# Optimization experiments

Measured on AMD Instinct MI355X. Metric: run time of the kernel, lower is better.

Reference implementation:

```python
import jax, jax.numpy as jnp
import numpy as np

N_NODES = 100000
N_EDGES = 1600000
IN_DIM = 128
HEADS = 4
HEAD_DIM = 16  # hidden_dim 64 // 4 heads
HID = HEADS * HEAD_DIM
NEG_SLOPE = 0.2


def setup_inputs() -> dict:
    key = jax.random.key(0)
    ks = jax.random.split(key, 20)
    inp = {
        "x": jax.random.normal(ks[0], (N_NODES, IN_DIM), dtype=jnp.float32),
        "edge_index": jax.random.randint(ks[1], (2, N_EDGES), 0, N_NODES, dtype=jnp.int32),
    }
    dims = [IN_DIM, HID, HID]
    for l in range(3):
        d_in = dims[l]
        sc = 1.0 / np.sqrt(d_in)
        inp[f"w{l}"] = jax.random.normal(ks[2 + 4 * l], (d_in, HID), dtype=jnp.float32) * sc
        inp[f"asrc{l}"] = jax.random.normal(ks[3 + 4 * l], (HEADS, HEAD_DIM), dtype=jnp.float32) * 0.1
        inp[f"adst{l}"] = jax.random.normal(ks[4 + 4 * l], (HEADS, HEAD_DIM), dtype=jnp.float32) * 0.1
        inp[f"b{l}"] = jnp.zeros((HID,), dtype=jnp.float32)
    inp["out_w"] = jax.random.normal(ks[14], (HID, 1), dtype=jnp.float32) * (1.0 / np.sqrt(HID))
    inp["out_b"] = jnp.zeros((1,), dtype=jnp.float32)
    return inp


def _gat_layer(h, src, dst, W, a_src, a_dst, b):
    # h: [N, d_in]; src/dst: [E'] (self-loops already appended)
    n = h.shape[0]
    xh = (h @ W).reshape(n, HEADS, HEAD_DIM)              # [N,H,C]
    al_s = jnp.sum(xh * a_src, axis=-1)                   # [N,H]
    al_d = jnp.sum(xh * a_dst, axis=-1)                   # [N,H]
    e = jax.nn.leaky_relu(al_s[src] + al_d[dst], NEG_SLOPE)  # [E',H]
    # segment-softmax over incoming edges of each destination node
    m = jax.ops.segment_max(e, dst, num_segments=n)       # [N,H]
    p = jnp.exp(e - m[dst])
    z = jax.ops.segment_sum(p, dst, num_segments=n)       # [N,H]
    alpha = p / (z[dst] + 1e-16)                          # [E',H]
    msg = xh[src] * alpha[:, :, None]                     # [E',H,C]
    out = jax.ops.segment_sum(msg, dst, num_segments=n)   # [N,H,C]
    return out.reshape(n, HID) + b


def reference(x, edge_index, w0, asrc0, adst0, b0, w1, asrc1, adst1, b1,
              w2, asrc2, adst2, b2, out_w, out_b):
    n = x.shape[0]
    loops = jnp.arange(n, dtype=edge_index.dtype)
    src = jnp.concatenate([edge_index[0], loops])  # PyG GATConv adds self-loops
    dst = jnp.concatenate([edge_index[1], loops])
    h = x
    params = [(w0, asrc0, adst0, b0), (w1, asrc1, adst1, b1), (w2, asrc2, adst2, b2)]
    for W, a_s, a_d, b in params:
        h = _gat_layer(h, src, dst, W, a_s, a_d, b)
        h = jax.nn.relu(h)
    return (h @ out_w + out_b).squeeze(-1)  # [N]
```

## Files before the change

kernel.cpp:

```cpp
#include <hip/hip_runtime.h>


#define NBMAX 512
#define SCHUNK 4096
#define BCAP 8192
#define PADSLACK 768

typedef __attribute__((ext_vector_type(8))) short bf16x8;
typedef __attribute__((ext_vector_type(4))) float f32x4;

__device__ inline unsigned short bf16_rtn(float x) {
    union { float f; unsigned u; } a; a.f = x;
    return (unsigned short)((a.u + 0x7FFFu + ((a.u >> 16) & 1u)) >> 16);
}
__device__ inline float bf16_to_f(unsigned short s) {
    union { unsigned u; float f; } b; b.u = ((unsigned)s) << 16;
    return b.f;
}

__global__ __launch_bounds__(256) void k_init(int* __restrict__ bhist, int nb,
                                              float* __restrict__ als, float* __restrict__ xh, int n) {
    int i = blockIdx.x * 256 + threadIdx.x;
    if (i < nb) bhist[i] = 0;
    int j = i - NBMAX;
    if (j >= 0 && j < 4) als[(size_t)n * 4 + j] = -1e30f;
    int k = i - NBMAX - 4;
    if (k >= 0 && k < 64) xh[(size_t)n * 64 + k] = 0.f;
}

__global__ __launch_bounds__(256) void k_bhist(const int* __restrict__ dst, int* __restrict__ bhist, int e) {
    __shared__ unsigned int h[NBMAX];
    int t = threadIdx.x;
    h[t] = 0;
    h[t + 256] = 0;
    __syncthreads();
    for (int i = blockIdx.x * 256 + t; i < e; i += gridDim.x * 256)
        atomicAdd(&h[dst[i] >> 8], 1u);
    __syncthreads();
    if (h[t]) atomicAdd(&bhist[t], (int)h[t]);
    if (h[t + 256]) atomicAdd(&bhist[t + 256], (int)h[t + 256]);
}

__global__ __launch_bounds__(512) void k_bscan(const int* __restrict__ bhist, int* __restrict__ boffs,
                                               int* __restrict__ bfill, int nb, int e) {
    __shared__ int s[NBMAX];
    int t = threadIdx.x;
    int v = (t < nb) ? bhist[t] : 0;
    s[t] = v;
    __syncthreads();
    for (int o = 1; o < 512; o <<= 1) {
        int add = (t >= o) ? s[t - o] : 0;
        __syncthreads();
        s[t] += add;
        __syncthreads();
    }
    boffs[t] = s[t] - v;
    if (t == 511) boffs[512] = s[511];
    bfill[t] = 0;
}

__global__ __launch_bounds__(512) void k_bscatter(const int* __restrict__ src, const int* __restrict__ dst,
                                                  const int* __restrict__ boffs, int* __restrict__ bfill,
                                                  unsigned int* __restrict__ edata, int e) {
    __shared__ unsigned int hist[NBMAX];
    __shared__ unsigned int loc[NBMAX];
    __shared__ int gbase[NBMAX];
    __shared__ unsigned int stmp[NBMAX];
    __shared__ unsigned int sortbuf[SCHUNK];
    __shared__ int posbuf[SCHUNK];
    int t = threadIdx.x;
    int i0 = blockIdx.x * SCHUNK;
    int cnt = min(SCHUNK, e - i0);
    hist[t] = 0;
    __syncthreads();
    for (int j = t; j < cnt; j += 512) atomicAdd(&hist[dst[i0 + j] >> 8], 1u);
    __syncthreads();
    unsigned int v = hist[t];
    stmp[t] = v;
    __syncthreads();
    for (int o = 1; o < 512; o <<= 1) {
        unsigned int add = (t >= o) ? stmp[t - o] : 0;
        __syncthreads();
        stmp[t] += add;
        __syncthreads();
    }
    loc[t] = stmp[t] - v;
    int gb = 0;
    if (v > 0) gb = atomicAdd(&bfill[t], (int)v);
    gbase[t] = boffs[t] + gb - (int)loc[t];
    hist[t] = loc[t];
    __syncthreads();
    for (int j = t; j < cnt; j += 512) {
        int d = dst[i0 + j];
        int s = src[i0 + j];
        int b = d >> 8;
        unsigned int p = atomicAdd(&hist[b], 1u);
        sortbuf[p] = (unsigned int)s | ((unsigned int)(d & 255) << 24);
        posbuf[p] = gbase[b] + (int)p;
    }
    __syncthreads();
    for (int j = t; j < cnt; j += 512) edata[posbuf[j]] = sortbuf[j];
}

__global__ __launch_bounds__(256) void k_bfinal(const unsigned int* __restrict__ edata,
                                                const int* __restrict__ boffs, int* __restrict__ poffs,
                                                int* __restrict__ pend, int* __restrict__ ssrc,
                                                int n, int nb) {
    __shared__ unsigned int hist[256];
    __shared__ unsigned int stmp[256];
    __shared__ unsigned int loc[256];
    __shared__ unsigned int srcbuf[BCAP];
    int b = blockIdx.x;
    int t = threadIdx.x;
    int e0 = boffs[b], e1 = boffs[b + 1];
    int cnt = e1 - e0;
    int pb = e0 + b * PADSLACK;
    hist[t] = 0;
    __syncthreads();
    for (int j = t; j < cnt; j += 256) atomicAdd(&hist[edata[e0 + j] >> 24], 1u);
    __syncthreads();
    unsigned int v = hist[t];
    unsigned int v4 = (v + 3u) & ~3u;
    stmp[t] = v4;
    __syncthreads();
    for (int o = 1; o < 256; o <<= 1) {
        unsigned int add = (t >= o) ? stmp[t - o] : 0;
        __syncthreads();
        stmp[t] += add;
        __syncthreads();
    }
    loc[t] = stmp[t] - v4;
    int ptot = (int)stmp[255];
    int node = b * 256 + t;
    if (node < n) {
        poffs[node] = pb + (int)loc[t];
        pend[node] = pb + (int)(loc[t] + v4);
    }
    hist[t] = loc[t];
    __syncthreads();
    if (cnt + PADSLACK <= BCAP) {
        for (int j = t; j < cnt; j += 256) {
            unsigned int p = edata[e0 + j];
            unsigned int pos = atomicAdd(&hist[p >> 24], 1u);
            srcbuf[pos] = p & 0xFFFFFFu;
        }
        for (unsigned int k = v; k < v4; ++k) srcbuf[loc[t] + k] = (unsigned int)n;
        __syncthreads();
        for (int j = t; j < ptot; j += 256) ssrc[pb + j] = (int)srcbuf[j];
    } else {
        for (int j = t; j < cnt; j += 256) {
            unsigned int p = edata[e0 + j];
            unsigned int pos = atomicAdd(&hist[p >> 24], 1u);
            ssrc[pb + (int)pos] = (int)(p & 0xFFFFFFu);
        }
        for (unsigned int k = v; k < v4; ++k) ssrc[pb + (int)(loc[t] + k)] = n;
    }
}

__global__ __launch_bounds__(256) void k_wprep(const float* __restrict__ w0, const float* __restrict__ w1,
                                               const float* __restrict__ w2,
                                               unsigned short* __restrict__ p0h, unsigned short* __restrict__ p0l,
                                               unsigned short* __restrict__ p1h, unsigned short* __restrict__ p1l,
                                               unsigned short* __restrict__ p2h, unsigned short* __restrict__ p2l) {
    int g = blockIdx.x * 256 + threadIdx.x;
    const float* W;
    unsigned short *ph, *pl;
    int idx;
    if (g < 1024) { W = w0; ph = p0h; pl = p0l; idx = g; }
    else if (g < 1536) { W = w1; ph = p1h; pl = p1l; idx = g - 1024; }
    else if (g < 2048) { W = w2; ph = p2h; pl = p2l; idx = g - 1536; }
    else return;
    int ko = idx >> 6, nn = idx & 63;
#pragma unroll
    for (int j = 0; j < 8; ++j) {
        float w = W[(size_t)(ko * 8 + j) * 64 + nn];
        unsigned short hb = bf16_rtn(w);
        ph[(size_t)idx * 8 + j] = hb;
        pl[(size_t)idx * 8 + j] = bf16_rtn(w - bf16_to_f(hb));
    }
}

template <int D_IN>
__global__ __launch_bounds__(256) void k_mgemm(const float* __restrict__ h,
                                               const unsigned short* __restrict__ wph,
                                               const unsigned short* __restrict__ wpl,
                                               const float* __restrict__ asrc, const float* __restrict__ adst,
                                               float* __restrict__ xh, float* __restrict__ als,
                                               float* __restrict__ ald, float* __restrict__ mvec, int n) {
    int t = threadIdx.x;
    int wv = t >> 6, lane = t & 63;
    int quad = lane >> 4, l16 = lane & 15;
    int m0 = blockIdx.x * 64 + wv * 16;
    int node_a = m0 + l16;
    int mm = min(node_a, n - 1);
    const float* hrow = h + (size_t)mm * D_IN + quad * 8;

    f32x4 acc[4];
#pragma unroll
    for (int i = 0; i < 4; ++i) acc[i] = (f32x4){0.f, 0.f, 0.f, 0.f};

    constexpr int KSTEPS = D_IN / 32;
#pragma unroll
    for (int s = 0; s < KSTEPS; ++s) {
        float4 a0 = *(const float4*)(hrow + s * 32);
        float4 a1 = *(const float4*)(hrow + s * 32 + 4);
        float av[8] = {a0.x, a0.y, a0.z, a0.w, a1.x, a1.y, a1.z, a1.w};
        bf16x8 ahi, alo;
#pragma unroll
        for (int j = 0; j < 8; ++j) {
            unsigned short hb = bf16_rtn(av[j]);
            ahi[j] = (short)hb;
            alo[j] = (short)bf16_rtn(av[j] - bf16_to_f(hb));
        }
        const unsigned short* bbase = wph + ((size_t)((s * 4 + quad) * 64 + l16)) * 8;
        const unsigned short* bbasel = wpl + ((size_t)((s * 4 + quad) * 64 + l16)) * 8;
#pragma unroll
        for (int nt = 0; nt < 4; ++nt) {
            bf16x8 bhi = *(const bf16x8*)(bbase + (size_t)nt * 16 * 8);
            bf16x8 blo = *(const bf16x8*)(bbasel + (size_t)nt * 16 * 8);
            acc[nt] = __builtin_amdgcn_mfma_f32_16x16x32_bf16(ahi, bhi, acc[nt], 0, 0, 0);
            acc[nt] = __builtin_amdgcn_mfma_f32_16x16x32_bf16(ahi, blo, acc[nt], 0, 0, 0);
            acc[nt] = __builtin_amdgcn_mfma_f32_16x16x32_bf16(alo, bhi, acc[nt], 0, 0, 0);
        }
    }
#pragma unroll
    for (int nt = 0; nt < 4; ++nt) {
        float as_l = asrc[nt * 16 + l16];
        float ad_l = adst[nt * 16 + l16];
#pragma unroll
        for (int r = 0; r < 4; ++r) {
            int node = m0 + quad * 4 + r;
            float c = acc[nt][r];
            if (node < n) xh[(size_t)node * 64 + nt * 16 + l16] = c;
            float ps = c * as_l, pd = c * ad_l;
            ps += __shfl_xor(ps, 1, 64); pd += __shfl_xor(pd, 1, 64);
            ps += __shfl_xor(ps, 2, 64); pd += __shfl_xor(pd, 2, 64);
            ps += __shfl_xor(ps, 4, 64); pd += __shfl_xor(pd, 4, 64);
            ps += __shfl_xor(ps, 8, 64); pd += __shfl_xor(pd, 8, 64);
            if (l16 == 0 && node < n) {
                als[node * 4 + nt] = ps;
                ald[node * 4 + nt] = pd;
                float sm = ps + pd;
                mvec[node * 4 + nt] = sm >= 0.f ? sm : 0.2f * sm;
            }
        }
    }
}

__device__ inline float4 lrelu4(float4 v) {
    float4 r;
    r.x = v.x >= 0.f ? v.x : 0.2f * v.x;
    r.y = v.y >= 0.f ? v.y : 0.2f * v.y;
    r.z = v.z >= 0.f ? v.z : 0.2f * v.z;
    r.w = v.w >= 0.f ? v.w : 0.2f * v.w;
    return r;
}

#define ACCUM(LO, HI, ACCA, ACCB, ZS)                                           \
    {                                                                           \
        int g_ = ((LO) - s0) >> 2, gb_ = ((HI) - s0) >> 2;                      \
        for (; g_ + 4 <= gb_; g_ += 4) {                                        \
            int4 uu0 = *(const int4*)&ub[g_ * 4];                               \
            int4 uu1 = *(const int4*)&ub[g_ * 4 + 4];                           \
            int4 uu2 = *(const int4*)&ub[g_ * 4 + 8];                           \
            int4 uu3 = *(const int4*)&ub[g_ * 4 + 12];                          \
            float4 pp0 = *(const float4*)&per[g_ * 4];                          \
            float4 pp1 = *(const float4*)&per[g_ * 4 + 4];                      \
            float4 pp2 = *(const float4*)&per[g_ * 4 + 8];                      \
            float4 pp3 = *(const float4*)&per[g_ * 4 + 12];                     \
            float x0 = *(const float*)(xl + (size_t)(unsigned)uu0.x);           \
            float x1 = *(const float*)(xl + (size_t)(unsigned)uu0.y);           \
            float x2 = *(const float*)(xl + (size_t)(unsigned)uu0.z);           \
            float x3 = *(const float*)(xl + (size_t)(unsigned)uu0.w);           \
            float x4 = *(const float*)(xl + (size_t)(unsigned)uu1.x);           \
            float x5 = *(const float*)(xl + (size_t)(unsigned)uu1.y);           \
            float x6 = *(const float*)(xl + (size_t)(unsigned)uu1.z);           \
            float x7 = *(const float*)(xl + (size_t)(unsigned)uu1.w);           \
            float x8 = *(const float*)(xl + (size_t)(unsigned)uu2.x);           \
            float x9 = *(const float*)(xl + (size_t)(unsigned)uu2.y);           \
            float xa = *(const float*)(xl + (size_t)(unsigned)uu2.z);           \
            float xb = *(const float*)(xl + (size_t)(unsigned)uu2.w);           \
            float xc = *(const float*)(xl + (size_t)(unsigned)uu3.x);           \
            float xd = *(const float*)(xl + (size_t)(unsigned)uu3.y);           \
            float xe = *(const float*)(xl + (size_t)(unsigned)uu3.z);           \
            float xf = *(const float*)(xl + (size_t)(unsigned)uu3.w);           \
            ZS += pp0.x + pp0.y + pp0.z + pp0.w;                                \
            ZS += pp1.x + pp1.y + pp1.z + pp1.w;                                \
            ZS += pp2.x + pp2.y + pp2.z + pp2.w;                                \
            ZS += pp3.x + pp3.y + pp3.z + pp3.w;                                \
            ACCA += pp0.x * x0; ACCB += pp0.y * x1;                             \
            ACCA += pp0.z * x2; ACCB += pp0.w * x3;                             \
            ACCA += pp1.x * x4; ACCB += pp1.y * x5;                             \
            ACCA += pp1.z * x6; ACCB += pp1.w * x7;                             \
            ACCA += pp2.x * x8; ACCB += pp2.y * x9;                             \
            ACCA += pp2.z * xa; ACCB += pp2.w * xb;                             \
            ACCA += pp3.x * xc; ACCB += pp3.y * xd;                             \
            ACCA += pp3.z * xe; ACCB += pp3.w * xf;                             \
        }                                                                       \
        for (; g_ < gb_; ++g_) {                                                \
            int4 uu = *(const int4*)&ub[g_ * 4];                                \
            float4 pp = *(const float4*)&per[g_ * 4];                           \
            float x0 = *(const float*)(xl + (size_t)(unsigned)uu.x);            \
            float x1 = *(const float*)(xl + (size_t)(unsigned)uu.y);            \
            float x2 = *(const float*)(xl + (size_t)(unsigned)uu.z);            \
            float x3 = *(const float*)(xl + (size_t)(unsigned)uu.w);            \
            ZS += pp.x + pp.y + pp.z + pp.w;                                    \
            ACCA += pp.x * x0; ACCB += pp.y * x1;                               \
            ACCA += pp.z * x2; ACCB += pp.w * x3;                               \
        }                                                                       \
    }

__global__ __launch_bounds__(256) void k_agg(const float* __restrict__ xh,
                                             const float* __restrict__ als, const float* __restrict__ ald,
                                             const float* __restrict__ mvec,
                                             const int* __restrict__ poffs, const int* __restrict__ pend,
                                             const int* __restrict__ ssrc,
                                             const float* __restrict__ bias, float* __restrict__ hout,
                                             const float* __restrict__ outw, const float* __restrict__ outb,
                                             float* __restrict__ fout, int n) {
    __shared__ int s_u[4][64];
    __shared__ float s_pe[4][4][64];
    int wslot = threadIdx.x >> 6;
    int lane = threadIdx.x & 63;
    int w = (blockIdx.x * 256 + threadIdx.x) >> 6;
    int v0 = w << 2;
    if (v0 >= n) return;
    int head = lane >> 4;
    int* ub = s_u[wslot];
    float* per = s_pe[wslot][head];
    float* pew = &s_pe[wslot][0][lane];

    int vlast = n - 1;
    int last = min(v0 + 3, vlast);
    int4 rr = *(const int4*)(poffs + v0);
    int e3 = pend[last];
    int r0 = rr.x;
    int r1 = (v0 + 1 <= last) ? rr.y : e3;
    int r2 = (v0 + 2 <= last) ? rr.z : e3;
    int r3 = (v0 + 3 <= last) ? rr.w : e3;

    const char* xl = (const char*)(xh + lane);
    float acc0a = *(const float*)(xl + ((size_t)(unsigned)v0 << 8));
    float acc1a = *(const float*)(xl + ((size_t)(unsigned)min(v0 + 1, vlast) << 8));
    float acc2a = *(const float*)(xl + ((size_t)(unsigned)min(v0 + 2, vlast) << 8));
    float acc3a = *(const float*)(xl + ((size_t)(unsigned)min(v0 + 3, vlast) << 8));
    float acc0b = 0.f, acc1b = 0.f, acc2b = 0.f, acc3b = 0.f;
    float zs0 = 0.f, zs1 = 0.f, zs2 = 0.f, zs3 = 0.f;

    int s0 = r0;
    int u_n = n;
    if (s0 < e3) {
        if (lane < e3 - s0) u_n = ssrc[s0 + lane];
    }
    float4 alu_n = *(const float4*)(als + 4 * (size_t)u_n);
    int e_n = s0 + lane;
    int nid_n = min(v0 + (e_n >= r1) + (e_n >= r2) + (e_n >= r3), vlast);
    float4 ald_n = *(const float4*)(ald + 4 * (size_t)nid_n);
    float4 m_n = *(const float4*)(mvec + 4 * (size_t)nid_n);

    while (s0 < e3) {
        int cnt = min(64, e3 - s0);
        float4 e4 = lrelu4(make_float4(alu_n.x + ald_n.x, alu_n.y + ald_n.y,
                                       alu_n.z + ald_n.z, alu_n.w + ald_n.w));
        float4 pe;
        pe.x = __expf(e4.x - m_n.x);
        pe.y = __expf(e4.y - m_n.y);
        pe.z = __expf(e4.z - m_n.z);
        pe.w = __expf(e4.w - m_n.w);
        ub[lane] = u_n << 8;
        pew[0] = pe.x;
        pew[64] = pe.y;
        pew[128] = pe.z;
        pew[192] = pe.w;
        int s1 = s0 + 64;
        if (s1 < e3) {
            u_n = n;
            if (lane < e3 - s1) u_n = ssrc[s1 + lane];
            alu_n = *(const float4*)(als + 4 * (size_t)u_n);
            int e1 = s1 + lane;
            int nid1 = min(v0 + (e1 >= r1) + (e1 >= r2) + (e1 >= r3), vlast);
            ald_n = *(const float4*)(ald + 4 * (size_t)nid1);
            m_n = *(const float4*)(mvec + 4 * (size_t)nid1);
        }
        int lim = s0 + cnt;
        int hi0 = min(r1, lim);
        int lo1 = max(r1, s0), hi1 = min(r2, lim);
        int lo2 = max(r2, s0), hi2 = min(r3, lim);
        int lo3 = max(r3, s0);
        ACCUM(s0, hi0, acc0a, acc0b, zs0);
        ACCUM(lo1, hi1, acc1a, acc1b, zs1);
        ACCUM(lo2, hi2, acc2a, acc2b, zs2);
        ACCUM(lo3, lim, acc3a, acc3b, zs3);
        s0 = s1;
    }

    float bl = bias[lane];
    float o0 = fmaxf((acc0a + acc0b) / (1.f + zs0 + 1e-16f) + bl, 0.f);
    float o1 = fmaxf((acc1a + acc1b) / (1.f + zs1 + 1e-16f) + bl, 0.f);
    float o2 = fmaxf((acc2a + acc2b) / (1.f + zs2 + 1e-16f) + bl, 0.f);
    float o3 = fmaxf((acc3a + acc3b) / (1.f + zs3 + 1e-16f) + bl, 0.f);
    if (outw) {
        float ow = outw[lane];
        float ob = outb[0];
        float t0 = o0 * ow, t1 = o1 * ow, t2 = o2 * ow, t3 = o3 * ow;
#pragma unroll
        for (int d = 32; d; d >>= 1) {
            t0 += __shfl_down(t0, d, 64);
            t1 += __shfl_down(t1, d, 64);
            t2 += __shfl_down(t2, d, 64);
            t3 += __shfl_down(t3, d, 64);
        }
        if (lane == 0) {
            fout[v0] = t0 + ob;
            if (v0 + 1 < n) fout[v0 + 1] = t1 + ob;
            if (v0 + 2 < n) fout[v0 + 2] = t2 + ob;
            if (v0 + 3 < n) fout[v0 + 3] = t3 + ob;
        }
    } else {
        hout[((size_t)v0 << 6) + lane] = o0;
        if (v0 + 1 < n) hout[((size_t)(v0 + 1) << 6) + lane] = o1;
        if (v0 + 2 < n) hout[((size_t)(v0 + 2) << 6) + lane] = o2;
        if (v0 + 3 < n) hout[((size_t)(v0 + 3) << 6) + lane] = o3;
    }
}

extern "C" void kernel_launch(void* const* d_in, const int* in_sizes, int n_in,
                              void* d_out, int out_size, void* d_ws, size_t ws_size,
                              hipStream_t stream) {
    const float* x = (const float*)d_in[0];
    const int* ei = (const int*)d_in[1];
    const float* w[3] = {(const float*)d_in[2], (const float*)d_in[6], (const float*)d_in[10]};
    const float* as[3] = {(const float*)d_in[3], (const float*)d_in[7], (const float*)d_in[11]};
    const float* ad[3] = {(const float*)d_in[4], (const float*)d_in[8], (const float*)d_in[12]};
    const float* b[3] = {(const float*)d_in[5], (const float*)d_in[9], (const float*)d_in[13]};
    const float* outw = (const float*)d_in[14];
    const float* outb = (const float*)d_in[15];

    const int N = in_sizes[0] / 128;
    const int E = in_sizes[1] / 2;
    const int* src = ei;
    const int* dst = ei + E;
    const int NB = (N + 255) / 256;

    char* ws = (char*)d_ws;
    auto alloc = [&](size_t bytes) -> void* {
        void* p = (void*)ws;
        ws += (bytes + 255) & ~(size_t)255;
        return p;
    };
    int* bhist = (int*)alloc(NBMAX * 4);
    int* boffs = (int*)alloc((NBMAX + 1) * 4);
    int* bfill = (int*)alloc(NBMAX * 4);
    int* poffs = (int*)alloc((size_t)(N + 8) * 4);
    int* pend = (int*)alloc((size_t)N * 4);
    int* ssrc = (int*)alloc((size_t)(E + NBMAX * PADSLACK + 256) * 4);
    float* xh = (float*)alloc((size_t)(N + 1) * 64 * 4);
    float* hbuf = (float*)alloc((size_t)N * 64 * 4);
    float* als = (float*)alloc((size_t)(N + 1) * 4 * 4);
    float* ald = (float*)alloc((size_t)N * 4 * 4);
    float* mvec = (float*)alloc((size_t)N * 4 * 4);
    unsigned short* p0h = (unsigned short*)alloc(8192 * 2);
    unsigned short* p0l = (unsigned short*)alloc(8192 * 2);
    unsigned short* p1h = (unsigned short*)alloc(4096 * 2);
    unsigned short* p1l = (unsigned short*)alloc(4096 * 2);
    unsigned short* p2h = (unsigned short*)alloc(4096 * 2);
    unsigned short* p2l = (unsigned short*)alloc(4096 * 2);
    unsigned int* edata = (unsigned int*)xh;

    k_wprep<<<8, 256, 0, stream>>>(w[0], w[1], w[2], p0h, p0l, p1h, p1l, p2h, p2l);
    k_init<<<3, 256, 0, stream>>>(bhist, NBMAX, als, xh, N);
    k_bhist<<<256, 256, 0, stream>>>(dst, bhist, E);
    k_bscan<<<1, 512, 0, stream>>>(bhist, boffs, bfill, NB, E);
    k_bscatter<<<(E + SCHUNK - 1) / SCHUNK, 512, 0, stream>>>(src, dst, boffs, bfill, edata, E);
    k_bfinal<<<NB, 256, 0, stream>>>(edata, boffs, poffs, pend, ssrc, N, NB);

    const int gblocks = (N + 63) / 64;
    const int ablocks = (N + 15) / 16;

    k_mgemm<128><<<gblocks, 256, 0, stream>>>(x, p0h, p0l, as[0], ad[0], xh, als, ald, mvec, N);
    k_agg<<<ablocks, 256, 0, stream>>>(xh, als, ald, mvec, poffs, pend, ssrc, b[0], hbuf, nullptr, nullptr, nullptr, N);
    k_mgemm<64><<<gblocks, 256, 0, stream>>>(hbuf, p1h, p1l, as[1], ad[1], xh, als, ald, mvec, N);
    k_agg<<<ablocks, 256, 0, stream>>>(xh, als, ald, mvec, poffs, pend, ssrc, b[1], hbuf, nullptr, nullptr, nullptr, N);
    k_mgemm<64><<<gblocks, 256, 0, stream>>>(hbuf, p2h, p2l, as[2], ad[2], xh, als, ald, mvec, N);
    k_agg<<<ablocks, 256, 0, stream>>>(xh, als, ald, mvec, poffs, pend, ssrc, b[2], nullptr, outw, outb, (float*)d_out, N);
}
```

Before: 435.4 us.

## Overlap layer-0 GEMM with CSR build by co-launching in mixed kernels

Merges weight prep and init into one kernel and splits the layer-0 projection GEMM across the two edge-sort kernels (bucket scatter and bucket finalize) as extra blocks, so independent GEMM work overlaps the sort phases. edata gets its own buffer instead of aliasing xh, because xh is now written concurrently. The finalize kernel moves to 512 threads to match the shared launch, and the GEMM blocks cover 128 nodes with 8 waves. This trades fewer launches and better overlap for a larger workspace and blocks carrying the sort kernels' shared memory footprint.

```diff
diff --git a/kernel.cpp b/kernel.cpp
--- a/kernel.cpp
+++ b/kernel.cpp
@@ -18,151 +18,22 @@
     return b.f;
 }
 
-__global__ __launch_bounds__(256) void k_init(int* __restrict__ bhist, int nb,
-                                              float* __restrict__ als, float* __restrict__ xh, int n) {
-    int i = blockIdx.x * 256 + threadIdx.x;
-    if (i < nb) bhist[i] = 0;
-    int j = i - NBMAX;
-    if (j >= 0 && j < 4) als[(size_t)n * 4 + j] = -1e30f;
-    int k = i - NBMAX - 4;
-    if (k >= 0 && k < 64) xh[(size_t)n * 64 + k] = 0.f;
-}
-
-__global__ __launch_bounds__(256) void k_bhist(const int* __restrict__ dst, int* __restrict__ bhist, int e) {
-    __shared__ unsigned int h[NBMAX];
-    int t = threadIdx.x;
-    h[t] = 0;
-    h[t + 256] = 0;
-    __syncthreads();
-    for (int i = blockIdx.x * 256 + t; i < e; i += gridDim.x * 256)
-        atomicAdd(&h[dst[i] >> 8], 1u);
-    __syncthreads();
-    if (h[t]) atomicAdd(&bhist[t], (int)h[t]);
-    if (h[t + 256]) atomicAdd(&bhist[t + 256], (int)h[t + 256]);
-}
-
-__global__ __launch_bounds__(512) void k_bscan(const int* __restrict__ bhist, int* __restrict__ boffs,
-                                               int* __restrict__ bfill, int nb, int e) {
-    __shared__ int s[NBMAX];
-    int t = threadIdx.x;
-    int v = (t < nb) ? bhist[t] : 0;
-    s[t] = v;
-    __syncthreads();
-    for (int o = 1; o < 512; o <<= 1) {
-        int add = (t >= o) ? s[t - o] : 0;
-        __syncthreads();
-        s[t] += add;
-        __syncthreads();
-    }
-    boffs[t] = s[t] - v;
-    if (t == 511) boffs[512] = s[511];
-    bfill[t] = 0;
-}
-
-__global__ __launch_bounds__(512) void k_bscatter(const int* __restrict__ src, const int* __restrict__ dst,
-                                                  const int* __restrict__ boffs, int* __restrict__ bfill,
-                                                  unsigned int* __restrict__ edata, int e) {
-    __shared__ unsigned int hist[NBMAX];
-    __shared__ unsigned int loc[NBMAX];
-    __shared__ int gbase[NBMAX];
-    __shared__ unsigned int stmp[NBMAX];
-    __shared__ unsigned int sortbuf[SCHUNK];
-    __shared__ int posbuf[SCHUNK];
-    int t = threadIdx.x;
-    int i0 = blockIdx.x * SCHUNK;
-    int cnt = min(SCHUNK, e - i0);
-    hist[t] = 0;
-    __syncthreads();
-    for (int j = t; j < cnt; j += 512) atomicAdd(&hist[dst[i0 + j] >> 8], 1u);
-    __syncthreads();
-    unsigned int v = hist[t];
-    stmp[t] = v;
-    __syncthreads();
-    for (int o = 1; o < 512; o <<= 1) {
-        unsigned int add = (t >= o) ? stmp[t - o] : 0;
-        __syncthreads();
-        stmp[t] += add;
-        __syncthreads();
-    }
-    loc[t] = stmp[t] - v;
-    int gb = 0;
-    if (v > 0) gb = atomicAdd(&bfill[t], (int)v);
-    gbase[t] = boffs[t] + gb - (int)loc[t];
-    hist[t] = loc[t];
-    __syncthreads();
-    for (int j = t; j < cnt; j += 512) {
-        int d = dst[i0 + j];
-        int s = src[i0 + j];
-        int b = d >> 8;
-        unsigned int p = atomicAdd(&hist[b], 1u);
-        sortbuf[p] = (unsigned int)s | ((unsigned int)(d & 255) << 24);
-        posbuf[p] = gbase[b] + (int)p;
-    }
-    __syncthreads();
-    for (int j = t; j < cnt; j += 512) edata[posbuf[j]] = sortbuf[j];
-}
-
-__global__ __launch_bounds__(256) void k_bfinal(const unsigned int* __restrict__ edata,
-                                                const int* __restrict__ boffs, int* __restrict__ poffs,
-                                                int* __restrict__ pend, int* __restrict__ ssrc,
-                                                int n, int nb) {
-    __shared__ unsigned int hist[256];
-    __shared__ unsigned int stmp[256];
-    __shared__ unsigned int loc[256];
-    __shared__ unsigned int srcbuf[BCAP];
-    int b = blockIdx.x;
-    int t = threadIdx.x;
-    int e0 = boffs[b], e1 = boffs[b + 1];
-    int cnt = e1 - e0;
-    int pb = e0 + b * PADSLACK;
-    hist[t] = 0;
-    __syncthreads();
-    for (int j = t; j < cnt; j += 256) atomicAdd(&hist[edata[e0 + j] >> 24], 1u);
-    __syncthreads();
-    unsigned int v = hist[t];
-    unsigned int v4 = (v + 3u) & ~3u;
-    stmp[t] = v4;
-    __syncthreads();
-    for (int o = 1; o < 256; o <<= 1) {
-        unsigned int add = (t >= o) ? stmp[t - o] : 0;
-        __syncthreads();
-        stmp[t] += add;
-        __syncthreads();
-    }
-    loc[t] = stmp[t] - v4;
-    int ptot = (int)stmp[255];
-    int node = b * 256 + t;
-    if (node < n) {
-        poffs[node] = pb + (int)loc[t];
-        pend[node] = pb + (int)(loc[t] + v4);
-    }
-    hist[t] = loc[t];
-    __syncthreads();
-    if (cnt + PADSLACK <= BCAP) {
-        for (int j = t; j < cnt; j += 256) {
-            unsigned int p = edata[e0 + j];
-            unsigned int pos = atomicAdd(&hist[p >> 24], 1u);
-            srcbuf[pos] = p & 0xFFFFFFu;
-        }
-        for (unsigned int k = v; k < v4; ++k) srcbuf[loc[t] + k] = (unsigned int)n;
-        __syncthreads();
-        for (int j = t; j < ptot; j += 256) ssrc[pb + j] = (int)srcbuf[j];
-    } else {
-        for (int j = t; j < cnt; j += 256) {
-            unsigned int p = edata[e0 + j];
-            unsigned int pos = atomicAdd(&hist[p >> 24], 1u);
-            ssrc[pb + (int)pos] = (int)(p & 0xFFFFFFu);
-        }
-        for (unsigned int k = v; k < v4; ++k) ssrc[pb + (int)(loc[t] + k)] = n;
-    }
-}
-
-__global__ __launch_bounds__(256) void k_wprep(const float* __restrict__ w0, const float* __restrict__ w1,
-                                               const float* __restrict__ w2,
-                                               unsigned short* __restrict__ p0h, unsigned short* __restrict__ p0l,
-                                               unsigned short* __restrict__ p1h, unsigned short* __restrict__ p1l,
-                                               unsigned short* __restrict__ p2h, unsigned short* __restrict__ p2l) {
-    int g = blockIdx.x * 256 + threadIdx.x;
+__global__ __launch_bounds__(256) void k_prep(const float* __restrict__ w0, const float* __restrict__ w1,
+                                              const float* __restrict__ w2,
+                                              unsigned short* __restrict__ p0h, unsigned short* __restrict__ p0l,
+                                              unsigned short* __restrict__ p1h, unsigned short* __restrict__ p1l,
+                                              unsigned short* __restrict__ p2h, unsigned short* __restrict__ p2l,
+                                              int* __restrict__ bhist, float* __restrict__ als,
+                                              float* __restrict__ xh, int n) {
+    int bid = blockIdx.x, t = threadIdx.x;
+    if (bid == 8) {
+        bhist[t] = 0;
+        bhist[t + 256] = 0;
+        if (t < 4) als[(size_t)n * 4 + t] = -1e30f;
+        if (t < 64) xh[(size_t)n * 64 + t] = 0.f;
+        return;
+    }
+    int g = bid * 256 + t;
     const float* W;
     unsigned short *ph, *pl;
     int idx;
@@ -180,17 +51,46 @@
     }
 }
 
+__global__ __launch_bounds__(256) void k_bhist(const int* __restrict__ dst, int* __restrict__ bhist, int e) {
+    __shared__ unsigned int h[NBMAX];
+    int t = threadIdx.x;
+    h[t] = 0;
+    h[t + 256] = 0;
+    __syncthreads();
+    for (int i = blockIdx.x * 256 + t; i < e; i += gridDim.x * 256)
+        atomicAdd(&h[dst[i] >> 8], 1u);
+    __syncthreads();
+    if (h[t]) atomicAdd(&bhist[t], (int)h[t]);
+    if (h[t + 256]) atomicAdd(&bhist[t + 256], (int)h[t + 256]);
+}
+
+__global__ __launch_bounds__(512) void k_bscan(const int* __restrict__ bhist, int* __restrict__ boffs,
+                                               int* __restrict__ bfill, int nb, int e) {
+    __shared__ int s[NBMAX];
+    int t = threadIdx.x;
+    int v = (t < nb) ? bhist[t] : 0;
+    s[t] = v;
+    __syncthreads();
+    for (int o = 1; o < 512; o <<= 1) {
+        int add = (t >= o) ? s[t - o] : 0;
+        __syncthreads();
+        s[t] += add;
+        __syncthreads();
+    }
+    boffs[t] = s[t] - v;
+    if (t == 511) boffs[512] = s[511];
+    bfill[t] = 0;
+}
+
 template <int D_IN>
-__global__ __launch_bounds__(256) void k_mgemm(const float* __restrict__ h,
-                                               const unsigned short* __restrict__ wph,
-                                               const unsigned short* __restrict__ wpl,
-                                               const float* __restrict__ asrc, const float* __restrict__ adst,
-                                               float* __restrict__ xh, float* __restrict__ als,
-                                               float* __restrict__ ald, float* __restrict__ mvec, int n) {
-    int t = threadIdx.x;
-    int wv = t >> 6, lane = t & 63;
+__device__ __forceinline__ void mgemm_wave(const float* __restrict__ h,
+                                           const unsigned short* __restrict__ wph,
+                                           const unsigned short* __restrict__ wpl,
+                                           const float* __restrict__ asrc, const float* __restrict__ adst,
+                                           float* __restrict__ xh, float* __restrict__ als,
+                                           float* __restrict__ ald, float* __restrict__ mvec,
+                                           int m0, int lane, int n) {
     int quad = lane >> 4, l16 = lane & 15;
-    int m0 = blockIdx.x * 64 + wv * 16;
     int node_a = m0 + l16;
     int mm = min(node_a, n - 1);
     const float* hrow = h + (size_t)mm * D_IN + quad * 8;
@@ -244,6 +144,148 @@
                 mvec[node * 4 + nt] = sm >= 0.f ? sm : 0.2f * sm;
             }
         }
+    }
+}
+
+template <int D_IN>
+__global__ __launch_bounds__(256) void k_mgemm(const float* __restrict__ h,
+                                               const unsigned short* __restrict__ wph,
+                                               const unsigned short* __restrict__ wpl,
+                                               const float* __restrict__ asrc, const float* __restrict__ adst,
+                                               float* __restrict__ xh, float* __restrict__ als,
+                                               float* __restrict__ ald, float* __restrict__ mvec, int n) {
+    int t = threadIdx.x;
+    int m0 = blockIdx.x * 64 + (t >> 6) * 16;
+    mgemm_wave<D_IN>(h, wph, wpl, asrc, adst, xh, als, ald, mvec, m0, t & 63, n);
+}
+
+__global__ __launch_bounds__(512) void k_mix1(const int* __restrict__ src, const int* __restrict__ dst,
+                                              const int* __restrict__ boffs, int* __restrict__ bfill,
+                                              unsigned int* __restrict__ edata, int e, int sb,
+                                              const float* __restrict__ x,
+                                              const unsigned short* __restrict__ p0h,
+                                              const unsigned short* __restrict__ p0l,
+                                              const float* __restrict__ asrc, const float* __restrict__ adst,
+                                              float* __restrict__ xh, float* __restrict__ als,
+                                              float* __restrict__ ald, float* __restrict__ mvec, int n) {
+    __shared__ unsigned int hist[NBMAX];
+    __shared__ unsigned int loc[NBMAX];
+    __shared__ int gbase[NBMAX];
+    __shared__ unsigned int stmp[NBMAX];
+    __shared__ unsigned int sortbuf[SCHUNK];
+    __shared__ int posbuf[SCHUNK];
+    int t = threadIdx.x;
+    if (blockIdx.x >= sb) {
+        int mblk = blockIdx.x - sb;
+        int m0 = mblk * 128 + (t >> 6) * 16;
+        mgemm_wave<128>(x, p0h, p0l, asrc, adst, xh, als, ald, mvec, m0, t & 63, n);
+        return;
+    }
+    int i0 = blockIdx.x * SCHUNK;
+    int cnt = min(SCHUNK, e - i0);
+    hist[t] = 0;
+    __syncthreads();
+    for (int j = t; j < cnt; j += 512) atomicAdd(&hist[dst[i0 + j] >> 8], 1u);
+    __syncthreads();
+    unsigned int v = hist[t];
+    stmp[t] = v;
+    __syncthreads();
+    for (int o = 1; o < 512; o <<= 1) {
+        unsigned int add = (t >= o) ? stmp[t - o] : 0;
+        __syncthreads();
+        stmp[t] += add;
+        __syncthreads();
+    }
+    loc[t] = stmp[t] - v;
+    int gb = 0;
+    if (v > 0) gb = atomicAdd(&bfill[t], (int)v);
+    gbase[t] = boffs[t] + gb - (int)loc[t];
+    hist[t] = loc[t];
+    __syncthreads();
+    for (int j = t; j < cnt; j += 512) {
+        int d = dst[i0 + j];
+        int s = src[i0 + j];
+        int b = d >> 8;
+        unsigned int p = atomicAdd(&hist[b], 1u);
+        sortbuf[p] = (unsigned int)s | ((unsigned int)(d & 255) << 24);
+        posbuf[p] = gbase[b] + (int)p;
+    }
+    __syncthreads();
+    for (int j = t; j < cnt; j += 512) edata[posbuf[j]] = sortbuf[j];
+}
+
+__global__ __launch_bounds__(512) void k_mix2(const unsigned int* __restrict__ edata,
+                                              const int* __restrict__ boffs, int* __restrict__ poffs,
+                                              int* __restrict__ pend, int* __restrict__ ssrc,
+                                              int n, int nb, int mg1,
+                                              const float* __restrict__ x,
+                                              const unsigned short* __restrict__ p0h,
+                                              const unsigned short* __restrict__ p0l,
+                                              const float* __restrict__ asrc, const float* __restrict__ adst,
+                                              float* __restrict__ xh, float* __restrict__ als,
+                                              float* __restrict__ ald, float* __restrict__ mvec) {
+    __shared__ unsigned int hist[256];
+    __shared__ unsigned int stmp[256];
+    __shared__ unsigned int loc2[256];
+    __shared__ unsigned int srcbuf[BCAP];
+    int t = threadIdx.x;
+    if (blockIdx.x >= nb) {
+        int mblk = mg1 + (blockIdx.x - nb);
+        int m0 = mblk * 128 + (t >> 6) * 16;
+        mgemm_wave<128>(x, p0h, p0l, asrc, adst, xh, als, ald, mvec, m0, t & 63, n);
+        return;
+    }
+    int b = blockIdx.x;
+    int e0 = boffs[b], e1 = boffs[b + 1];
+    int cnt = e1 - e0;
+    int pb = e0 + b * PADSLACK;
+    if (t < 256) hist[t] = 0;
+    __syncthreads();
+    for (int j = t; j < cnt; j += 512) atomicAdd(&hist[edata[e0 + j] >> 24], 1u);
+    __syncthreads();
+    unsigned int v = 0, v4 = 0;
+    if (t < 256) {
+        v = hist[t];
+        v4 = (v + 3u) & ~3u;
+        stmp[t] = v4;
+    }
+    __syncthreads();
+    for (int o = 1; o < 256; o <<= 1) {
+        unsigned int add = 0;
+        if (t < 256 && t >= o) add = stmp[t - o];
+        __syncthreads();
+        if (t < 256) stmp[t] += add;
+        __syncthreads();
+    }
+    int ptot = (int)stmp[255];
+    if (t < 256) {
+        loc2[t] = stmp[t] - v4;
+        int node = b * 256 + t;
+        if (node < n) {
+            poffs[node] = pb + (int)loc2[t];
+            pend[node] = pb + (int)(loc2[t] + v4);
+        }
+        hist[t] = loc2[t];
+    }
+    __syncthreads();
+    if (cnt + PADSLACK <= BCAP) {
+        for (int j = t; j < cnt; j += 512) {
+            unsigned int p = edata[e0 + j];
+            unsigned int pos = atomicAdd(&hist[p >> 24], 1u);
+            srcbuf[pos] = p & 0xFFFFFFu;
+        }
+        if (t < 256)
+            for (unsigned int k = v; k < v4; ++k) srcbuf[loc2[t] + k] = (unsigned int)n;
+        __syncthreads();
+        for (int j = t; j < ptot; j += 512) ssrc[pb + j] = (int)srcbuf[j];
+    } else {
+        for (int j = t; j < cnt; j += 512) {
+            unsigned int p = edata[e0 + j];
+            unsigned int pos = atomicAdd(&hist[p >> 24], 1u);
+            ssrc[pb + (int)pos] = (int)(p & 0xFFFFFFu);
+        }
+        if (t < 256)
+            for (unsigned int k = v; k < v4; ++k) ssrc[pb + (int)(loc2[t] + k)] = n;
     }
 }
 
@@ -441,6 +483,10 @@
     const int* src = ei;
     const int* dst = ei + E;
     const int NB = (N + 255) / 256;
+    const int SB = (E + SCHUNK - 1) / SCHUNK;
+    const int GB128 = (N + 127) / 128;
+    const int MG1 = (GB128 + 1) / 2;
+    const int MG2 = GB128 - MG1;
 
     char* ws = (char*)d_ws;
     auto alloc = [&](size_t bytes) -> void* {
@@ -454,6 +500,7 @@
     int* poffs = (int*)alloc((size_t)(N + 8) * 4);
     int* pend = (int*)alloc((size_t)N * 4);
     int* ssrc = (int*)alloc((size_t)(E + NBMAX * PADSLACK + 256) * 4);
+    unsigned int* edata = (unsigned int*)alloc((size_t)(E + 64) * 4);
     float* xh = (float*)alloc((size_t)(N + 1) * 64 * 4);
     float* hbuf = (float*)alloc((size_t)N * 64 * 4);
     float* als = (float*)alloc((size_t)(N + 1) * 4 * 4);
@@ -465,19 +512,18 @@
     unsigned short* p1l = (unsigned short*)alloc(4096 * 2);
     unsigned short* p2h = (unsigned short*)alloc(4096 * 2);
     unsigned short* p2l = (unsigned short*)alloc(4096 * 2);
-    unsigned int* edata = (unsigned int*)xh;
-
-    k_wprep<<<8, 256, 0, stream>>>(w[0], w[1], w[2], p0h, p0l, p1h, p1l, p2h, p2l);
-    k_init<<<3, 256, 0, stream>>>(bhist, NBMAX, als, xh, N);
+
+    k_prep<<<9, 256, 0, stream>>>(w[0], w[1], w[2], p0h, p0l, p1h, p1l, p2h, p2l, bhist, als, xh, N);
     k_bhist<<<256, 256, 0, stream>>>(dst, bhist, E);
     k_bscan<<<1, 512, 0, stream>>>(bhist, boffs, bfill, NB, E);
-    k_bscatter<<<(E + SCHUNK - 1) / SCHUNK, 512, 0, stream>>>(src, dst, boffs, bfill, edata, E);
-    k_bfinal<<<NB, 256, 0, stream>>>(edata, boffs, poffs, pend, ssrc, N, NB);
+    k_mix1<<<SB + MG1, 512, 0, stream>>>(src, dst, boffs, bfill, edata, E, SB,
+                                         x, p0h, p0l, as[0], ad[0], xh, als, ald, mvec, N);
+    k_mix2<<<NB + MG2, 512, 0, stream>>>(edata, boffs, poffs, pend, ssrc, N, NB, MG1,
+                                         x, p0h, p0l, as[0], ad[0], xh, als, ald, mvec);
 
     const int gblocks = (N + 63) / 64;
     const int ablocks = (N + 15) / 16;
 
-    k_mgemm<128><<<gblocks, 256, 0, stream>>>(x, p0h, p0l, as[0], ad[0], xh, als, ald, mvec, N);
     k_agg<<<ablocks, 256, 0, stream>>>(xh, als, ald, mvec, poffs, pend, ssrc, b[0], hbuf, nullptr, nullptr, nullptr, N);
     k_mgemm<64><<<gblocks, 256, 0, stream>>>(hbuf, p1h, p1l, as[1], ad[1], xh, als, ald, mvec, N);
     k_agg<<<ablocks, 256, 0, stream>>>(xh, als, ald, mvec, poffs, pend, ssrc, b[1], hbuf, nullptr, nullptr, nullptr, N);
```

Result: faster. 426.6 us (-2.0%).
